# Optimization experiments

Measured on AMD Instinct MI355X. Metric: run time of the kernel, lower is better.

## Reference

```python
import jax, jax.numpy as jnp
import numpy as np

D = 1024      # dim_input
H = 16        # n_heads
DH = 64       # dim_inner
S = 1024      # current_seq
M = 1024      # pre_seq (memory)
B = 2         # batch
SCALE = 1.0 / np.sqrt(DH)


def _rel_shift(x):
    # x: [S, J, B, H]; Transformer-XL relative shift
    s, j = x.shape[0], x.shape[1]
    zero = jnp.zeros((s, 1) + x.shape[2:], x.dtype)
    x = jnp.concatenate([zero, x], axis=1)            # [S, J+1, B, H]
    x = x.reshape((j + 1, s) + x.shape[2:])[1:]        # [J, S, B, H]
    return x.reshape((s, j) + x.shape[2:])             # [S, J, B, H]


def setup_inputs() -> dict:
    key = jax.random.key(0)
    ks = jax.random.split(key, 9)
    std = 1.0 / np.sqrt(D)
    return {
        "multi_head_input": jax.random.normal(ks[0], (S, B, D), jnp.float32),
        "position_emb": jax.random.normal(ks[1], (S + M, D), jnp.float32),
        "memory": jax.random.normal(ks[2], (M, B, D), jnp.float32),
        "u": jax.random.normal(ks[3], (H, DH), jnp.float32) * 0.02,
        "v": jax.random.normal(ks[4], (H, DH), jnp.float32) * 0.02,
        "W_kv": jax.random.normal(ks[5], (D, 2 * H * DH), jnp.float32) * std,
        "W_q": jax.random.normal(ks[6], (D, H * DH), jnp.float32) * std,
        "W_pos": jax.random.normal(ks[7], (D, H * DH), jnp.float32) * std,
        "W_out": jax.random.normal(ks[8], (H * DH, D), jnp.float32) * std,
    }


def reference(multi_head_input, position_emb, memory, u, v, W_kv, W_q, W_pos, W_out):
    s = multi_head_input.shape[0]
    m = memory.shape[0]
    b = multi_head_input.shape[1]
    x_mem = jnp.concatenate([memory, multi_head_input], axis=0)   # [M+S, B, D]
    kv = x_mem @ W_kv                                              # [M+S, B, 2*H*DH]
    k, val = jnp.split(kv, 2, axis=-1)
    k = k.reshape(m + s, b, H, DH)
    val = val.reshape(m + s, b, H, DH)
    q = (multi_head_input @ W_q).reshape(s, b, H, DH)              # [S, B, H, DH]

    # content term: (q + u) . k
    content = jnp.einsum('ibhd,jbhd->ijbh', q + u, k)              # [S, M+S, B, H]
    # position term: (q + v) . r, then rel_shift
    r = (position_emb @ W_pos).reshape(m + s, H, DH)               # [M+S, H, DH]
    pos = jnp.einsum('ibhd,jhd->ijbh', q + v, r)                   # [S, M+S, B, H]
    pos = _rel_shift(pos)

    attn = jax.nn.softmax((content + pos) * SCALE, axis=1)         # [S, M+S, B, H]
    out = jnp.einsum('ijbh,jbhd->ibhd', attn, val).reshape(s, b, H * DH)
    return out @ W_out                                             # [S, B, D]
```

## Files before the change

### kernel.cpp

```cpp
#include <hip/hip_runtime.h>
#include <hip/hip_bf16.h>
#include <hip/hip_fp16.h>
#include <math.h>

#define D    1024
#define H    16
#define DH   64
#define S    1024
#define M    1024
#define B    2
#define J    2048
#define SCALE 0.125f
#define SCALE_L2E 0.18033688f

typedef __attribute__((ext_vector_type(8))) short        bf16x8;
typedef __attribute__((ext_vector_type(4))) short        s16x4;
typedef __attribute__((ext_vector_type(8))) _Float16     h16x8;
typedef __attribute__((ext_vector_type(4))) _Float16     h16x4;
typedef __attribute__((ext_vector_type(8))) unsigned short us8;
typedef __attribute__((ext_vector_type(4))) unsigned short us4;
typedef __attribute__((ext_vector_type(4))) float        f32x4;

__device__ __forceinline__ short f2bs(float f) {
    __hip_bfloat16 t = __float2bfloat16(f);
    short r; __builtin_memcpy(&r, &t, 2); return r;
}
__device__ __forceinline__ unsigned short f2bf_fast(float f) {
    unsigned int u; __builtin_memcpy(&u, &f, 4);
    return (unsigned short)((u + 0x8000u) >> 16);
}

__device__ __forceinline__ void g2l16(const short* g, short* l) {
    __builtin_amdgcn_global_load_lds(
        (const __attribute__((address_space(1))) unsigned int*)g,
        (__attribute__((address_space(3))) unsigned int*)l, 16, 0, 0);
}

__global__ __launch_bounds__(256)
void prep(const float* __restrict__ mem, const float* __restrict__ x,
          const float* __restrict__ pemb,
          const float* __restrict__ Wkv, const float* __restrict__ Wq,
          const float* __restrict__ Wpos, const float* __restrict__ Wout,
          short* __restrict__ a_bf, short* __restrict__ p_bf,
          short* __restrict__ wkvt, short* __restrict__ wqt,
          short* __restrict__ wpt,  short* __restrict__ wot)
{
    __shared__ float t[64][65];
    int blk = blockIdx.x;
    const int tid = threadIdx.x;
    if (blk < 6144) {
        const int idx = (blk * 256 + tid) * 4;
        const int TWO_M = 2 * 1024 * 1024;
        float4 v; short* dst;
        if (idx < TWO_M)          { v = *(const float4*)(mem  + idx);           dst = a_bf + idx; }
        else if (idx < 2 * TWO_M) { v = *(const float4*)(x    + idx - TWO_M);   dst = a_bf + idx; }
        else                      { v = *(const float4*)(pemb + idx - 2*TWO_M); dst = p_bf + idx - 2*TWO_M; }
        s16x4 o = { f2bs(v.x), f2bs(v.y), f2bs(v.z), f2bs(v.w) };
        *(s16x4*)dst = o;
        return;
    }
    blk -= 6144;
    const float* src; short* dst; int N, t0;
    if (blk < 512)       { src = Wkv;  dst = wkvt; N = 2048; t0 = blk; }
    else if (blk < 768)  { src = Wq;   dst = wqt;  N = 1024; t0 = blk - 512; }
    else if (blk < 1024) { src = Wpos; dst = wpt;  N = 1024; t0 = blk - 768; }
    else                 { src = Wout; dst = wot;  N = 1024; t0 = blk - 1024; }
    const int ntn = N >> 6;
    const int k0 = (t0 / ntn) * 64, n0 = (t0 % ntn) * 64;
    #pragma unroll
    for (int e = tid; e < 4096; e += 256) {
        int r = e >> 6, c = e & 63;
        t[r][c] = src[(size_t)(k0 + r) * N + n0 + c];
    }
    __syncthreads();
    #pragma unroll
    for (int e = tid; e < 4096; e += 256) {
        int nr = e >> 6, kc = e & 63;
        dst[(size_t)(n0 + nr) * 1024 + k0 + kc] = f2bs(t[kc][nr]);
    }
}

__device__ __forceinline__ void gemm_core(const short* __restrict__ A,
                                          const short* __restrict__ Bt,
                                          short* As, short* Bs,
                                          int bm0, int bn0, int tid,
                                          f32x4 acc[4][4])
{
    const int w    = tid >> 6;
    const int wy   = w >> 1, wx = w & 1;
    const int lane = tid & 63;
    const int lm   = lane & 15;
    const int lq   = lane >> 4;

    for (int k0 = 0; k0 < 1024; k0 += 64) {
        const short* Ab = A  + (size_t)bm0 * 1024 + k0;
        const short* Bb = Bt + (size_t)bn0 * 1024 + k0;
        #pragma unroll
        for (int t = 0; t < 4; ++t) {
            int s = t * 256 + tid;
            int r = s >> 3, c = s & 7;
            int cg = c ^ (r & 7);
            g2l16(Ab + r * 1024 + cg * 8, As + s * 8);
            g2l16(Bb + r * 1024 + cg * 8, Bs + s * 8);
        }
        __syncthreads();
        #pragma unroll
        for (int kk = 0; kk < 2; ++kk) {
            bf16x8 af[4], bg[4];
            #pragma unroll
            for (int r4 = 0; r4 < 4; ++r4) {
                int ar = wy * 64 + r4 * 16 + lm;
                int kc = kk * 4 + lq;
                af[r4] = *(const bf16x8*)(As + ((ar << 3) + (kc ^ (ar & 7))) * 8);
            }
            #pragma unroll
            for (int c4 = 0; c4 < 4; ++c4) {
                int br = wx * 64 + c4 * 16 + lm;
                int kc = kk * 4 + lq;
                bg[c4] = *(const bf16x8*)(Bs + ((br << 3) + (kc ^ (br & 7))) * 8);
            }
            #pragma unroll
            for (int r4 = 0; r4 < 4; ++r4)
                #pragma unroll
                for (int c4 = 0; c4 < 4; ++c4)
                    acc[r4][c4] = __builtin_amdgcn_mfma_f32_16x16x32_bf16(
                        af[r4], bg[c4], acc[r4][c4], 0, 0, 0);
        }
        __syncthreads();
    }
}

__global__ __launch_bounds__(256)
void proj_fused(const short* __restrict__ a_bf, const short* __restrict__ p_bf,
                const short* __restrict__ wkvt, const short* __restrict__ wqt,
                const short* __restrict__ wpt,
                short* __restrict__ k_bf, short* __restrict__ vt_bf,
                short* __restrict__ qu_bf, short* __restrict__ qv_bf,
                short* __restrict__ r_bf,
                const float* __restrict__ uvec, const float* __restrict__ vvec)
{
    __shared__ __align__(16) short As[128 * 64];
    __shared__ __align__(16) short Bs[128 * 64];

    int blk = (blockIdx.x & 7) * 96 + (blockIdx.x >> 3);

    int mode, bx, by;
    const short *A, *Bt;
    if (blk < 512)      { bx = blk & 15; by = blk >> 4;
                          if (bx >= 8) { mode = 4; A = wkvt; Bt = a_bf; }
                          else         { mode = 0; A = a_bf; Bt = wkvt; } }
    else if (blk < 640) { int b2 = blk - 512; mode = 1; bx = b2 & 7; by = b2 >> 3;
                          A = a_bf + (size_t)2048 * 1024; Bt = wqt; }
    else                { int b3 = blk - 640; mode = 2; bx = b3 & 7; by = b3 >> 3;
                          A = p_bf; Bt = wpt; }
    const int bn0 = (mode == 4) ? by * 128 : bx * 128;
    const int bm0 = (mode == 4) ? bx * 128 : by * 128;
    const int tid = threadIdx.x;
    const int w = tid >> 6, wy = w >> 1, wx = w & 1;
    const int lane = tid & 63, lm = lane & 15, lq = lane >> 4;

    f32x4 acc[4][4];
    #pragma unroll
    for (int r = 0; r < 4; ++r)
        #pragma unroll
        for (int c = 0; c < 4; ++c) acc[r][c] = (f32x4){0.f, 0.f, 0.f, 0.f};

    gemm_core(A, Bt, As, Bs, bm0, bn0, tid, acc);

    #pragma unroll
    for (int r4 = 0; r4 < 4; ++r4) {
        #pragma unroll
        for (int c4 = 0; c4 < 4; ++c4) {
            const int n = bn0 + wx * 64 + c4 * 16 + lm;
            float ubias = 0.f, vbias = 0.f;
            if (mode == 1) { ubias = uvec[n]; vbias = vvec[n]; }
            #pragma unroll
            for (int reg = 0; reg < 4; ++reg) {
                const int m = bm0 + wy * 64 + r4 * 16 + lq * 4 + reg;
                const float val = acc[r4][c4][reg];
                if (mode == 0) {
                    int j = m >> 1, b = m & 1;
                    int h = n >> 6, d = n & 63;
                    k_bf[(((size_t)b * H + h) * J + j) * DH + d] = f2bs(val);
                } else if (mode == 4) {
                    int n2 = m - 1024, h = n2 >> 6, d = n2 & 63;
                    int j = n >> 1, b = n & 1;
                    vt_bf[(((size_t)b * H + h) * DH + d) * J + j] = f2bs(val);
                } else if (mode == 1) {
                    int i = m >> 1, b = m & 1;
                    int h = n >> 6, d = n & 63;
                    size_t o = (((size_t)b * H + h) * S + i) * DH + d;
                    qu_bf[o] = f2bs((val + ubias) * SCALE_L2E);
                    qv_bf[o] = f2bs((val + vbias) * SCALE_L2E);
                } else {
                    int h = n >> 6, d = n & 63;
                    r_bf[((size_t)h * J + m) * DH + d] = f2bs(val);
                }
            }
        }
    }
}

__global__ __launch_bounds__(256)
void gemm_out(const short* __restrict__ A, const short* __restrict__ Bt,
              float* __restrict__ out)
{
    __shared__ __align__(16) short As[64 * 64];
    __shared__ __align__(16) short Bs[128 * 64];
    const int bn0 = blockIdx.x * 128, bm0 = blockIdx.y * 64;
    const int tid = threadIdx.x;
    const int w = tid >> 6;
    const int lane = tid & 63, lm = lane & 15, lq = lane >> 4;

    f32x4 acc[4][2];
    #pragma unroll
    for (int r = 0; r < 4; ++r)
        #pragma unroll
        for (int c = 0; c < 2; ++c) acc[r][c] = (f32x4){0.f, 0.f, 0.f, 0.f};

    for (int k0 = 0; k0 < 1024; k0 += 64) {
        const short* Ab = A  + (size_t)bm0 * 1024 + k0;
        const short* Bb = Bt + (size_t)bn0 * 1024 + k0;
        #pragma unroll
        for (int t = 0; t < 2; ++t) {
            int s = t * 256 + tid;
            int r = s >> 3, c = s & 7;
            int cg = c ^ (r & 7);
            g2l16(Ab + r * 1024 + cg * 8, As + s * 8);
        }
        #pragma unroll
        for (int t = 0; t < 4; ++t) {
            int s = t * 256 + tid;
            int r = s >> 3, c = s & 7;
            int cg = c ^ (r & 7);
            g2l16(Bb + r * 1024 + cg * 8, Bs + s * 8);
        }
        __syncthreads();
        #pragma unroll
        for (int kk = 0; kk < 2; ++kk) {
            bf16x8 af[4], bg[2];
            #pragma unroll
            for (int r4 = 0; r4 < 4; ++r4) {
                int ar = r4 * 16 + lm;
                int kc = kk * 4 + lq;
                af[r4] = *(const bf16x8*)(As + ((ar << 3) + (kc ^ (ar & 7))) * 8);
            }
            #pragma unroll
            for (int c4 = 0; c4 < 2; ++c4) {
                int br = w * 32 + c4 * 16 + lm;
                int kc = kk * 4 + lq;
                bg[c4] = *(const bf16x8*)(Bs + ((br << 3) + (kc ^ (br & 7))) * 8);
            }
            #pragma unroll
            for (int r4 = 0; r4 < 4; ++r4)
                #pragma unroll
                for (int c4 = 0; c4 < 2; ++c4)
                    acc[r4][c4] = __builtin_amdgcn_mfma_f32_16x16x32_bf16(
                        af[r4], bg[c4], acc[r4][c4], 0, 0, 0);
        }
        __syncthreads();
    }

    #pragma unroll
    for (int r4 = 0; r4 < 4; ++r4)
        #pragma unroll
        for (int c4 = 0; c4 < 2; ++c4) {
            const int n = bn0 + w * 32 + c4 * 16 + lm;
            #pragma unroll
            for (int reg = 0; reg < 4; ++reg) {
                const int m = bm0 + r4 * 16 + lq * 4 + reg;
                out[(size_t)m * 1024 + n] = acc[r4][c4][reg];
            }
        }
}

__device__ __forceinline__ int sidx(int m, int c) {
    return (m << 10) + (c ^ (m << 3));
}

__global__ __launch_bounds__(512)
void attn_mfma(const short* __restrict__ qu_bf, const short* __restrict__ qv_bf,
               const short* __restrict__ k_bf,  const short* __restrict__ vt_bf,
               const short* __restrict__ r_bf,
               float* __restrict__ opart, float* __restrict__ ml)
{
    __shared__ unsigned short sc[32 * 1024];
    __shared__ float wsum[16][2][8];
    __half* sch = (__half*)sc;
    float*  scF = (float*)sc;

    const int L   = blockIdx.x;
    const int xcd = L & 7;
    const int pp  = L >> 3;
    const int bh  = (xcd << 2) + (pp >> 6);
    const int sub = pp & 63;
    const int it  = sub >> 1;
    const int jh  = sub & 1;

    const int i0  = it * 32;
    const int cbeg = jh << 10, cend = cbeg + 1024;
    const int h   = bh & (H - 1);
    const int tid = threadIdx.x;
    const int w    = tid >> 6;
    const int lane = tid & 63;
    const int lm   = lane & 15;
    const int lq   = lane >> 4;
    const int slot = (it * 32 + bh) * 2 + jh;

    const short* qup0 = qu_bf + ((size_t)(bh * S + i0 + lm)) * DH + lq * 8;
    const short* qup1 = qup0 + 16 * DH;
    bf16x8 au00 = *(const bf16x8*)qup0,        au01 = *(const bf16x8*)(qup0 + 32);
    bf16x8 au10 = *(const bf16x8*)qup1,        au11 = *(const bf16x8*)(qup1 + 32);
    const short* qvp0 = qv_bf + ((size_t)(bh * S + i0 + lm)) * DH + lq * 8;
    const short* qvp1 = qvp0 + 16 * DH;
    bf16x8 av00 = *(const bf16x8*)qvp0,        av01 = *(const bf16x8*)(qvp0 + 32);
    bf16x8 av10 = *(const bf16x8*)qvp1,        av11 = *(const bf16x8*)(qvp1 + 32);
    int r1a = i0 + 1 + lm;  if (r1a > S - 1) r1a = S - 1;
    int r1b = i0 + 17 + lm; if (r1b > S - 1) r1b = S - 1;
    const short* qwp0 = qv_bf + ((size_t)(bh * S + r1a)) * DH + lq * 8;
    const short* qwp1 = qv_bf + ((size_t)(bh * S + r1b)) * DH + lq * 8;
    bf16x8 aw00 = *(const bf16x8*)qwp0,        aw01 = *(const bf16x8*)(qwp0 + 32);
    bf16x8 aw10 = *(const bf16x8*)qwp1,        aw11 = *(const bf16x8*)(qwp1 + 32);

    if (tid < 32) {
        int hole = i0 + tid + 1025;
        if (hole >= cbeg && hole < cend) sc[sidx(tid, hole - cbeg)] = 0;
    }

    const short* rbase = r_bf + (size_t)h * J * DH;

    {
        int tmp = cbeg + 977 - i0;
        int tlo = tmp > 0 ? ((tmp + 15) >> 4) : 0;
        int thi = (cend + 1022 - i0) >> 4; if (thi > 127) thi = 127;
        int t = tlo + w;
        if (t <= thi) {
            const short* rp = rbase + (size_t)(t * 16 + lm) * DH + lq * 8;
            bf16x8 b0 = *(const bf16x8*)rp, b1 = *(const bf16x8*)(rp + 32);
            bf16x8 p0, p1;
            if (t + 8 <= thi) {
                const short* rp2 = rbase + (size_t)((t + 8) * 16 + lm) * DH + lq * 8;
                p0 = *(const bf16x8*)rp2; p1 = *(const bf16x8*)(rp2 + 32);
            }
            for (; t <= thi; t += 8) {
                bf16x8 n0, n1;
                if (t + 16 <= thi) {
                    const short* rpn = rbase + (size_t)((t + 16) * 16 + lm) * DH + lq * 8;
                    n0 = *(const bf16x8*)rpn; n1 = *(const bf16x8*)(rpn + 32);
                }
                f32x4 c0 = {0.f,0.f,0.f,0.f}, c1 = {0.f,0.f,0.f,0.f};
                __builtin_amdgcn_s_setprio(1);
                c0 = __builtin_amdgcn_mfma_f32_16x16x32_bf16(av00, b0, c0, 0, 0, 0);
                c1 = __builtin_amdgcn_mfma_f32_16x16x32_bf16(av10, b0, c1, 0, 0, 0);
                c0 = __builtin_amdgcn_mfma_f32_16x16x32_bf16(av01, b1, c0, 0, 0, 0);
                c1 = __builtin_amdgcn_mfma_f32_16x16x32_bf16(av11, b1, c1, 0, 0, 0);
                __builtin_amdgcn_s_setprio(0);
                int cb = i0 + t * 16 + lm - 1023 - cbeg;
                int base = i0 + 16 * t - 1023;
                if (base >= cbeg && base + 46 < cend) {
                    #pragma unroll
                    for (int r = 0; r < 4; ++r) {
                        int m0 = lq * 4 + r, m1 = m0 + 16;
                        sch[sidx(m0, cb + m0)] = __float2half(c0[r]);
                        sch[sidx(m1, cb + m1)] = __float2half(c1[r]);
                    }
                } else {
                    #pragma unroll
                    for (int r = 0; r < 4; ++r) {
                        int m0 = lq * 4 + r, m1 = m0 + 16;
                        int cA = cb + m0, cB = cb + m1;
                        if (cA >= 0 && cA < 1024) sch[sidx(m0, cA)] = __float2half(c0[r]);
                        if (cB >= 0 && cB < 1024) sch[sidx(m1, cB)] = __float2half(c1[r]);
                    }
                }
                b0 = p0; b1 = p1; p0 = n0; p1 = n1;
            }
        }
    }

    {
        int tmpw = cbeg - 1072 - i0;
        int tlw = tmpw > 0 ? ((tmpw + 15) >> 4) : 0;
        int thw = (cend - 1027 - i0) >> 4; if (thw > 127) thw = 127;
        int t = tlw + w;
        if (t <= thw) {
            const short* rp = rbase + (size_t)(t * 16 + lm) * DH + lq * 8;
            bf16x8 b0 = *(const bf16x8*)rp, b1 = *(const bf16x8*)(rp + 32);
            bf16x8 p0, p1;
            if (t + 8 <= thw) {
                const short* rp2 = rbase + (size_t)((t + 8) * 16 + lm) * DH + lq * 8;
                p0 = *(const bf16x8*)rp2; p1 = *(const bf16x8*)(rp2 + 32);
            }
            for (; t <= thw; t += 8) {
                bf16x8 n0, n1;
                if (t + 16 <= thw) {
                    const short* rpn = rbase + (size_t)((t + 16) * 16 + lm) * DH + lq * 8;
                    n0 = *(const bf16x8*)rpn; n1 = *(const bf16x8*)(rpn + 32);
                }
                f32x4 c0 = {0.f,0.f,0.f,0.f}, c1 = {0.f,0.f,0.f,0.f};
                __builtin_amdgcn_s_setprio(1);
                c0 = __builtin_amdgcn_mfma_f32_16x16x32_bf16(aw00, b0, c0, 0, 0, 0);
                c1 = __builtin_amdgcn_mfma_f32_16x16x32_bf16(aw10, b0, c1, 0, 0, 0);
                c0 = __builtin_amdgcn_mfma_f32_16x16x32_bf16(aw01, b1, c0, 0, 0, 0);
                c1 = __builtin_amdgcn_mfma_f32_16x16x32_bf16(aw11, b1, c1, 0, 0, 0);
                __builtin_amdgcn_s_setprio(0);
                int cb = i0 + t * 16 + lm + 1026 - cbeg;
                int base = i0 + 16 * t + 1026;
                if (base >= cbeg && base + 46 < cend) {
                    #pragma unroll
                    for (int r = 0; r < 4; ++r) {
                        int m0 = lq * 4 + r, m1 = m0 + 16;
                        sch[sidx(m0, cb + m0)] = __float2half(c0[r]);
                        sch[sidx(m1, cb + m1)] = __float2half(c1[r]);
                    }
                } else {
                    #pragma unroll
                    for (int r = 0; r < 4; ++r) {
                        int m0 = lq * 4 + r, m1 = m0 + 16;
                        int cA = cb + m0, cB = cb + m1;
                        if (cA >= 0 && cA < 1024) sch[sidx(m0, cA)] = __float2half(c0[r]);
                        if (cB >= 0 && cB < 1024) sch[sidx(m1, cB)] = __float2half(c1[r]);
                    }
                }
                b0 = p0; b1 = p1; p0 = n0; p1 = n1;
            }
        }
    }

    const short* kbase = k_bf + (size_t)bh * J * DH;
    bf16x8 kb0, kb1, kc0, kc1;
    {
        int t0 = jh * 64 + w + 8 * ((it) & 7);
        int t1 = jh * 64 + w + 8 * ((1 + it) & 7);
        const short* kp0 = kbase + (size_t)(t0 * 16 + lm) * DH + lq * 8;
        const short* kp1 = kbase + (size_t)(t1 * 16 + lm) * DH + lq * 8;
        kb0 = *(const bf16x8*)kp0; kb1 = *(const bf16x8*)(kp0 + 32);
        kc0 = *(const bf16x8*)kp1; kc1 = *(const bf16x8*)(kp1 + 32);
    }
    __syncthreads();

    float sum0 = 0.f, sum1 = 0.f;
    #pragma unroll 1
    for (int g = 0; g < 8; ++g) {
        bf16x8 nb0, nb1;
        if (g + 2 < 8) {
            int u = jh * 64 + w + 8 * ((g + 2 + it) & 7);
            const short* np = kbase + (size_t)(u * 16 + lm) * DH + lq * 8;
            nb0 = *(const bf16x8*)np; nb1 = *(const bf16x8*)(np + 32);
        }
        int t = jh * 64 + w + 8 * ((g + it) & 7);
        int lc = t * 16 - cbeg;
        int aA = sidx(lm,      lc + lq * 4);
        int aB = sidx(lm + 16, lc + lq * 4);
        h16x4 hA = *(const h16x4*)(sc + aA);
        h16x4 hB = *(const h16x4*)(sc + aB);
        f32x4 c0, c1;
        #pragma unroll
        for (int r = 0; r < 4; ++r) { c0[r] = (float)hA[r]; c1[r] = (float)hB[r]; }
        __builtin_amdgcn_s_setprio(1);
        c0 = __builtin_amdgcn_mfma_f32_16x16x32_bf16(kb0, au00, c0, 0, 0, 0);
        c1 = __builtin_amdgcn_mfma_f32_16x16x32_bf16(kb0, au10, c1, 0, 0, 0);
        c0 = __builtin_amdgcn_mfma_f32_16x16x32_bf16(kb1, au01, c0, 0, 0, 0);
        c1 = __builtin_amdgcn_mfma_f32_16x16x32_bf16(kb1, au11, c1, 0, 0, 0);
        __builtin_amdgcn_s_setprio(0);
        us4 oA, oB;
        #pragma unroll
        for (int r = 0; r < 4; ++r) {
            float e0 = __builtin_amdgcn_exp2f(c0[r]);
            float e1 = __builtin_amdgcn_exp2f(c1[r]);
            sum0 += e0; sum1 += e1;
            oA[r] = f2bf_fast(e0);
            oB[r] = f2bf_fast(e1);
        }
        *(us4*)(sc + aA) = oA;
        *(us4*)(sc + aB) = oB;
        kb0 = kc0; kb1 = kc1; kc0 = nb0; kc1 = nb1;
    }
    sum0 += __shfl_xor(sum0, 16); sum0 += __shfl_xor(sum0, 32);
    sum1 += __shfl_xor(sum1, 16); sum1 += __shfl_xor(sum1, 32);
    if (lane < 16) { wsum[lane][0][w] = sum0; wsum[lane][1][w] = sum1; }

    const int dslice = w & 3, jq = w >> 2;
    const short* vtb = vt_bf + ((size_t)bh * DH + dslice * 16 + lm) * J + cbeg + jq * 512;
    bf16x8 cv0, cv1, cv2, cv3;
    {
        int j0 = (it & 3) * 128;
        cv0 = *(const bf16x8*)(vtb + j0 +  0 + lq * 8);
        cv1 = *(const bf16x8*)(vtb + j0 + 32 + lq * 8);
        cv2 = *(const bf16x8*)(vtb + j0 + 64 + lq * 8);
        cv3 = *(const bf16x8*)(vtb + j0 + 96 + lq * 8);
    }
    __syncthreads();

    if (tid < 32) {
        float s = 0.f;
        #pragma unroll
        for (int ww = 0; ww < 8; ++ww) s += wsum[tid & 15][tid >> 4][ww];
        ml[(size_t)slot * 64 + tid * 2]     = 0.f;
        ml[(size_t)slot * 64 + tid * 2 + 1] = s;
    }

    f32x4 pa0 = {0.f,0.f,0.f,0.f}, pa1 = {0.f,0.f,0.f,0.f};
    f32x4 pa2 = {0.f,0.f,0.f,0.f}, pa3 = {0.f,0.f,0.f,0.f};
    f32x4 pb0 = {0.f,0.f,0.f,0.f}, pb1 = {0.f,0.f,0.f,0.f};
    f32x4 pb2 = {0.f,0.f,0.f,0.f}, pb3 = {0.f,0.f,0.f,0.f};
    #pragma unroll 1
    for (int jo0 = 0; jo0 < 4; ++jo0) {
        bf16x8 nv0, nv1, nv2, nv3;
        if (jo0 < 3) {
            int jn = ((jo0 + 1 + it) & 3) * 128;
            nv0 = *(const bf16x8*)(vtb + jn +  0 + lq * 8);
            nv1 = *(const bf16x8*)(vtb + jn + 32 + lq * 8);
            nv2 = *(const bf16x8*)(vtb + jn + 64 + lq * 8);
            nv3 = *(const bf16x8*)(vtb + jn + 96 + lq * 8);
        }
        int j0 = ((jo0 + it) & 3) * 128;
        int lb = jq * 512 + j0;
        bf16x8 a0 = *(const bf16x8*)(sc + sidx(lm, lb +  0 + lq * 8));
        bf16x8 a1 = *(const bf16x8*)(sc + sidx(lm, lb + 32 + lq * 8));
        bf16x8 a2 = *(const bf16x8*)(sc + sidx(lm, lb + 64 + lq * 8));
        bf16x8 a3 = *(const bf16x8*)(sc + sidx(lm, lb + 96 + lq * 8));
        bf16x8 c0 = *(const bf16x8*)(sc + sidx(16 + lm, lb +  0 + lq * 8));
        bf16x8 c1 = *(const bf16x8*)(sc + sidx(16 + lm, lb + 32 + lq * 8));
        bf16x8 c2 = *(const bf16x8*)(sc + sidx(16 + lm, lb + 64 + lq * 8));
        bf16x8 c3 = *(const bf16x8*)(sc + sidx(16 + lm, lb + 96 + lq * 8));
        __builtin_amdgcn_s_setprio(1);
        pa0 = __builtin_amdgcn_mfma_f32_16x16x32_bf16(a0, cv0, pa0, 0, 0, 0);
        pb0 = __builtin_amdgcn_mfma_f32_16x16x32_bf16(c0, cv0, pb0, 0, 0, 0);
        pa1 = __builtin_amdgcn_mfma_f32_16x16x32_bf16(a1, cv1, pa1, 0, 0, 0);
        pb1 = __builtin_amdgcn_mfma_f32_16x16x32_bf16(c1, cv1, pb1, 0, 0, 0);
        pa2 = __builtin_amdgcn_mfma_f32_16x16x32_bf16(a2, cv2, pa2, 0, 0, 0);
        pb2 = __builtin_amdgcn_mfma_f32_16x16x32_bf16(c2, cv2, pb2, 0, 0, 0);
        pa3 = __builtin_amdgcn_mfma_f32_16x16x32_bf16(a3, cv3, pa3, 0, 0, 0);
        pb3 = __builtin_amdgcn_mfma_f32_16x16x32_bf16(c3, cv3, pb3, 0, 0, 0);
        __builtin_amdgcn_s_setprio(0);
        if (jo0 < 3) { cv0 = nv0; cv1 = nv1; cv2 = nv2; cv3 = nv3; }
    }
    __syncthreads();

    #pragma unroll
    for (int r = 0; r < 4; ++r) {
        int m0 = lq * 4 + r, m1 = m0 + 16;
        scF[jq * 2048 + m0 * 64 + dslice * 16 + lm] = pa0[r] + pa1[r] + pa2[r] + pa3[r];
        scF[jq * 2048 + m1 * 64 + dslice * 16 + lm] = pb0[r] + pb1[r] + pb2[r] + pb3[r];
    }
    __syncthreads();

    float* op = opart + (size_t)slot * 2048;
    #pragma unroll
    for (int e = tid; e < 2048; e += 512)
        op[e] = scF[e] + scF[2048 + e];
}

__global__ __launch_bounds__(256)
void attn_combine(const float* __restrict__ opart, const float* __restrict__ ml,
                  short* __restrict__ o_bf)
{
    const int blk = blockIdx.x;
    const int it = blk >> 5, bh = blk & 31;
    const int h = bh & 15, bb = bh >> 4;
    __shared__ float wgt[32][2];
    const int tid = threadIdx.x;
    if (tid < 32) {
        float m0 = ml[(size_t)(blk * 2 + 0) * 64 + tid * 2];
        float l0 = ml[(size_t)(blk * 2 + 0) * 64 + tid * 2 + 1];
        float m1 = ml[(size_t)(blk * 2 + 1) * 64 + tid * 2];
        float l1 = ml[(size_t)(blk * 2 + 1) * 64 + tid * 2 + 1];
        float mx = fmaxf(m0, m1);
        float e0 = __expf(m0 - mx), e1 = __expf(m1 - mx);
        float inv = 1.0f / (e0 * l0 + e1 * l1);
        wgt[tid][0] = e0 * inv;
        wgt[tid][1] = e1 * inv;
    }
    __syncthreads();
    const float* p0 = opart + (size_t)(blk * 2 + 0) * 2048;
    const float* p1 = opart + (size_t)(blk * 2 + 1) * 2048;
    #pragma unroll
    for (int e4 = tid; e4 < 512; e4 += 256) {
        int e = e4 * 4;
        int m = e >> 6, d = e & 63;
        float4 a = *(const float4*)(p0 + e);
        float4 b = *(const float4*)(p1 + e);
        float w0 = wgt[m][0], w1 = wgt[m][1];
        s16x4 o = { f2bs(a.x * w0 + b.x * w1), f2bs(a.y * w0 + b.y * w1),
                    f2bs(a.z * w0 + b.z * w1), f2bs(a.w * w0 + b.w * w1) };
        *(s16x4*)(o_bf + ((size_t)(it * 32 + m) * B + bb) * (H * DH) + h * DH + d) = o;
    }
}

extern "C" void kernel_launch(void* const* d_in, const int* in_sizes, int n_in,
                              void* d_out, int out_size, void* d_ws, size_t ws_size,
                              hipStream_t stream)
{
    const float* x    = (const float*)d_in[0];
    const float* pemb = (const float*)d_in[1];
    const float* mem  = (const float*)d_in[2];
    const float* u    = (const float*)d_in[3];
    const float* v    = (const float*)d_in[4];
    const float* Wkv  = (const float*)d_in[5];
    const float* Wq   = (const float*)d_in[6];
    const float* Wpos = (const float*)d_in[7];
    const float* Wout = (const float*)d_in[8];
    float* out = (float*)d_out;

    char* p = (char*)d_ws;
    short* a_bf  = (short*)p; p += (size_t)4096 * 1024 * 2;
    short* p_bf  = (short*)p; p += (size_t)2048 * 1024 * 2;
    short* wkvt  = (short*)p; p += (size_t)2048 * 1024 * 2;
    short* wqt   = (short*)p; p += (size_t)1024 * 1024 * 2;
    short* wpt   = (short*)p; p += (size_t)1024 * 1024 * 2;
    short* wot   = (short*)p; p += (size_t)1024 * 1024 * 2;
    short* k_bf  = (short*)p; p += (size_t)B * H * J * DH * 2;
    short* vt_bf = (short*)p; p += (size_t)B * H * J * DH * 2;
    short* qu_bf = (short*)p; p += (size_t)B * H * S * DH * 2;
    short* qv_bf = (short*)p; p += (size_t)B * H * S * DH * 2;
    short* r_bf  = (short*)p; p += (size_t)H * J * DH * 2;
    short* o_bf  = (short*)p;

    float* opart = (float*)d_ws;
    float* ml    = (float*)((char*)d_ws + (size_t)16 * 1024 * 1024);

    prep<<<7424, 256, 0, stream>>>(mem, x, pemb, Wkv, Wq, Wpos, Wout,
                                   a_bf, p_bf, wkvt, wqt, wpt, wot);
    proj_fused<<<768, 256, 0, stream>>>(a_bf, p_bf, wkvt, wqt, wpt,
                                        k_bf, vt_bf, qu_bf, qv_bf, r_bf, u, v);
    attn_mfma<<<2048, 512, 0, stream>>>(
        qu_bf, qv_bf, k_bf, vt_bf, r_bf, opart, ml);
    attn_combine<<<(S / 32) * B * H, 256, 0, stream>>>(opart, ml, o_bf);
    gemm_out<<<dim3(8, 32), 256, 0, stream>>>(o_bf, wot, out);
}
```

Baseline: 283.9 us.

## Fuse split-J attention halves into one block, drop combine kernel, remap gemm_out

The attention kernel now loops over both halves of the key range inside each block, accumulating the PV products and exp sums in registers. It then normalizes and writes bf16 output directly, which removes the fp32 partial buffers and the separate combine kernel launch. The grid halves to 1024 blocks, so each block does twice the serial work and there is less parallelism for latency hiding. gemm_out also gets a 1D launch with a remapped block index so that blocks sharing rows are spread across XCDs.

Measured after the change: 279.9 us. About the same (-1.4%).

```diff
diff --git a/kernel.cpp b/kernel.cpp
--- a/kernel.cpp
+++ b/kernel.cpp
@@ -207,7 +207,8 @@
 {
     __shared__ __align__(16) short As[64 * 64];
     __shared__ __align__(16) short Bs[128 * 64];
-    const int bn0 = blockIdx.x * 128, bm0 = blockIdx.y * 64;
+    const int lb = (blockIdx.x & 7) * 32 + (blockIdx.x >> 3);
+    const int bn0 = (lb & 7) * 128, bm0 = (lb >> 3) * 64;
     const int tid = threadIdx.x;
     const int w = tid >> 6;
     const int lane = tid & 63, lm = lane & 15, lq = lane >> 4;
@@ -282,260 +283,258 @@
 void attn_mfma(const short* __restrict__ qu_bf, const short* __restrict__ qv_bf,
                const short* __restrict__ k_bf,  const short* __restrict__ vt_bf,
                const short* __restrict__ r_bf,
-               float* __restrict__ opart, float* __restrict__ ml)
+               short* __restrict__ o_bf)
 {
     __shared__ unsigned short sc[32 * 1024];
     __shared__ float wsum[16][2][8];
+    __shared__ float rtot[32];
     __half* sch = (__half*)sc;
     float*  scF = (float*)sc;
 
     const int L   = blockIdx.x;
     const int xcd = L & 7;
     const int pp  = L >> 3;
-    const int bh  = (xcd << 2) + (pp >> 6);
-    const int sub = pp & 63;
-    const int it  = sub >> 1;
-    const int jh  = sub & 1;
+    const int bh  = (xcd << 2) + (pp >> 5);
+    const int it  = pp & 31;
 
     const int i0  = it * 32;
-    const int cbeg = jh << 10, cend = cbeg + 1024;
     const int h   = bh & (H - 1);
     const int tid = threadIdx.x;
     const int w    = tid >> 6;
     const int lane = tid & 63;
     const int lm   = lane & 15;
     const int lq   = lane >> 4;
-    const int slot = (it * 32 + bh) * 2 + jh;
-
-    const short* qup0 = qu_bf + ((size_t)(bh * S + i0 + lm)) * DH + lq * 8;
-    const short* qup1 = qup0 + 16 * DH;
-    bf16x8 au00 = *(const bf16x8*)qup0,        au01 = *(const bf16x8*)(qup0 + 32);
-    bf16x8 au10 = *(const bf16x8*)qup1,        au11 = *(const bf16x8*)(qup1 + 32);
-    const short* qvp0 = qv_bf + ((size_t)(bh * S + i0 + lm)) * DH + lq * 8;
-    const short* qvp1 = qvp0 + 16 * DH;
-    bf16x8 av00 = *(const bf16x8*)qvp0,        av01 = *(const bf16x8*)(qvp0 + 32);
-    bf16x8 av10 = *(const bf16x8*)qvp1,        av11 = *(const bf16x8*)(qvp1 + 32);
-    int r1a = i0 + 1 + lm;  if (r1a > S - 1) r1a = S - 1;
-    int r1b = i0 + 17 + lm; if (r1b > S - 1) r1b = S - 1;
-    const short* qwp0 = qv_bf + ((size_t)(bh * S + r1a)) * DH + lq * 8;
-    const short* qwp1 = qv_bf + ((size_t)(bh * S + r1b)) * DH + lq * 8;
-    bf16x8 aw00 = *(const bf16x8*)qwp0,        aw01 = *(const bf16x8*)(qwp0 + 32);
-    bf16x8 aw10 = *(const bf16x8*)qwp1,        aw11 = *(const bf16x8*)(qwp1 + 32);
-
-    if (tid < 32) {
-        int hole = i0 + tid + 1025;
-        if (hole >= cbeg && hole < cend) sc[sidx(tid, hole - cbeg)] = 0;
-    }
+    const int dslice = w & 3, jq = w >> 2;
 
     const short* rbase = r_bf + (size_t)h * J * DH;
-
-    {
-        int tmp = cbeg + 977 - i0;
-        int tlo = tmp > 0 ? ((tmp + 15) >> 4) : 0;
-        int thi = (cend + 1022 - i0) >> 4; if (thi > 127) thi = 127;
-        int t = tlo + w;
-        if (t <= thi) {
-            const short* rp = rbase + (size_t)(t * 16 + lm) * DH + lq * 8;
-            bf16x8 b0 = *(const bf16x8*)rp, b1 = *(const bf16x8*)(rp + 32);
-            bf16x8 p0, p1;
-            if (t + 8 <= thi) {
-                const short* rp2 = rbase + (size_t)((t + 8) * 16 + lm) * DH + lq * 8;
-                p0 = *(const bf16x8*)rp2; p1 = *(const bf16x8*)(rp2 + 32);
-            }
-            for (; t <= thi; t += 8) {
-                bf16x8 n0, n1;
-                if (t + 16 <= thi) {
-                    const short* rpn = rbase + (size_t)((t + 16) * 16 + lm) * DH + lq * 8;
-                    n0 = *(const bf16x8*)rpn; n1 = *(const bf16x8*)(rpn + 32);
-                }
-                f32x4 c0 = {0.f,0.f,0.f,0.f}, c1 = {0.f,0.f,0.f,0.f};
-                __builtin_amdgcn_s_setprio(1);
-                c0 = __builtin_amdgcn_mfma_f32_16x16x32_bf16(av00, b0, c0, 0, 0, 0);
-                c1 = __builtin_amdgcn_mfma_f32_16x16x32_bf16(av10, b0, c1, 0, 0, 0);
-                c0 = __builtin_amdgcn_mfma_f32_16x16x32_bf16(av01, b1, c0, 0, 0, 0);
-                c1 = __builtin_amdgcn_mfma_f32_16x16x32_bf16(av11, b1, c1, 0, 0, 0);
-                __builtin_amdgcn_s_setprio(0);
-                int cb = i0 + t * 16 + lm - 1023 - cbeg;
-                int base = i0 + 16 * t - 1023;
-                if (base >= cbeg && base + 46 < cend) {
-                    #pragma unroll
-                    for (int r = 0; r < 4; ++r) {
-                        int m0 = lq * 4 + r, m1 = m0 + 16;
-                        sch[sidx(m0, cb + m0)] = __float2half(c0[r]);
-                        sch[sidx(m1, cb + m1)] = __float2half(c1[r]);
-                    }
-                } else {
-                    #pragma unroll
-                    for (int r = 0; r < 4; ++r) {
-                        int m0 = lq * 4 + r, m1 = m0 + 16;
-                        int cA = cb + m0, cB = cb + m1;
-                        if (cA >= 0 && cA < 1024) sch[sidx(m0, cA)] = __float2half(c0[r]);
-                        if (cB >= 0 && cB < 1024) sch[sidx(m1, cB)] = __float2half(c1[r]);
-                    }
-                }
-                b0 = p0; b1 = p1; p0 = n0; p1 = n1;
-            }
-        }
-    }
-
-    {
-        int tmpw = cbeg - 1072 - i0;
-        int tlw = tmpw > 0 ? ((tmpw + 15) >> 4) : 0;
-        int thw = (cend - 1027 - i0) >> 4; if (thw > 127) thw = 127;
-        int t = tlw + w;
-        if (t <= thw) {
-            const short* rp = rbase + (size_t)(t * 16 + lm) * DH + lq * 8;
-            bf16x8 b0 = *(const bf16x8*)rp, b1 = *(const bf16x8*)(rp + 32);
-            bf16x8 p0, p1;
-            if (t + 8 <= thw) {
-                const short* rp2 = rbase + (size_t)((t + 8) * 16 + lm) * DH + lq * 8;
-                p0 = *(const bf16x8*)rp2; p1 = *(const bf16x8*)(rp2 + 32);
-            }
-            for (; t <= thw; t += 8) {
-                bf16x8 n0, n1;
-                if (t + 16 <= thw) {
-                    const short* rpn = rbase + (size_t)((t + 16) * 16 + lm) * DH + lq * 8;
-                    n0 = *(const bf16x8*)rpn; n1 = *(const bf16x8*)(rpn + 32);
-                }
-                f32x4 c0 = {0.f,0.f,0.f,0.f}, c1 = {0.f,0.f,0.f,0.f};
-                __builtin_amdgcn_s_setprio(1);
-                c0 = __builtin_amdgcn_mfma_f32_16x16x32_bf16(aw00, b0, c0, 0, 0, 0);
-                c1 = __builtin_amdgcn_mfma_f32_16x16x32_bf16(aw10, b0, c1, 0, 0, 0);
-                c0 = __builtin_amdgcn_mfma_f32_16x16x32_bf16(aw01, b1, c0, 0, 0, 0);
-                c1 = __builtin_amdgcn_mfma_f32_16x16x32_bf16(aw11, b1, c1, 0, 0, 0);
-                __builtin_amdgcn_s_setprio(0);
-                int cb = i0 + t * 16 + lm + 1026 - cbeg;
-                int base = i0 + 16 * t + 1026;
-                if (base >= cbeg && base + 46 < cend) {
-                    #pragma unroll
-                    for (int r = 0; r < 4; ++r) {
-                        int m0 = lq * 4 + r, m1 = m0 + 16;
-                        sch[sidx(m0, cb + m0)] = __float2half(c0[r]);
-                        sch[sidx(m1, cb + m1)] = __float2half(c1[r]);
-                    }
-                } else {
-                    #pragma unroll
-                    for (int r = 0; r < 4; ++r) {
-                        int m0 = lq * 4 + r, m1 = m0 + 16;
-                        int cA = cb + m0, cB = cb + m1;
-                        if (cA >= 0 && cA < 1024) sch[sidx(m0, cA)] = __float2half(c0[r]);
-                        if (cB >= 0 && cB < 1024) sch[sidx(m1, cB)] = __float2half(c1[r]);
-                    }
-                }
-                b0 = p0; b1 = p1; p0 = n0; p1 = n1;
-            }
-        }
-    }
-
     const short* kbase = k_bf + (size_t)bh * J * DH;
-    bf16x8 kb0, kb1, kc0, kc1;
-    {
-        int t0 = jh * 64 + w + 8 * ((it) & 7);
-        int t1 = jh * 64 + w + 8 * ((1 + it) & 7);
-        const short* kp0 = kbase + (size_t)(t0 * 16 + lm) * DH + lq * 8;
-        const short* kp1 = kbase + (size_t)(t1 * 16 + lm) * DH + lq * 8;
-        kb0 = *(const bf16x8*)kp0; kb1 = *(const bf16x8*)(kp0 + 32);
-        kc0 = *(const bf16x8*)kp1; kc1 = *(const bf16x8*)(kp1 + 32);
-    }
-    __syncthreads();
 
     float sum0 = 0.f, sum1 = 0.f;
-    #pragma unroll 1
-    for (int g = 0; g < 8; ++g) {
-        bf16x8 nb0, nb1;
-        if (g + 2 < 8) {
-            int u = jh * 64 + w + 8 * ((g + 2 + it) & 7);
-            const short* np = kbase + (size_t)(u * 16 + lm) * DH + lq * 8;
-            nb0 = *(const bf16x8*)np; nb1 = *(const bf16x8*)(np + 32);
-        }
-        int t = jh * 64 + w + 8 * ((g + it) & 7);
-        int lc = t * 16 - cbeg;
-        int aA = sidx(lm,      lc + lq * 4);
-        int aB = sidx(lm + 16, lc + lq * 4);
-        h16x4 hA = *(const h16x4*)(sc + aA);
-        h16x4 hB = *(const h16x4*)(sc + aB);
-        f32x4 c0, c1;
-        #pragma unroll
-        for (int r = 0; r < 4; ++r) { c0[r] = (float)hA[r]; c1[r] = (float)hB[r]; }
-        __builtin_amdgcn_s_setprio(1);
-        c0 = __builtin_amdgcn_mfma_f32_16x16x32_bf16(kb0, au00, c0, 0, 0, 0);
-        c1 = __builtin_amdgcn_mfma_f32_16x16x32_bf16(kb0, au10, c1, 0, 0, 0);
-        c0 = __builtin_amdgcn_mfma_f32_16x16x32_bf16(kb1, au01, c0, 0, 0, 0);
-        c1 = __builtin_amdgcn_mfma_f32_16x16x32_bf16(kb1, au11, c1, 0, 0, 0);
-        __builtin_amdgcn_s_setprio(0);
-        us4 oA, oB;
-        #pragma unroll
-        for (int r = 0; r < 4; ++r) {
-            float e0 = __builtin_amdgcn_exp2f(c0[r]);
-            float e1 = __builtin_amdgcn_exp2f(c1[r]);
-            sum0 += e0; sum1 += e1;
-            oA[r] = f2bf_fast(e0);
-            oB[r] = f2bf_fast(e1);
-        }
-        *(us4*)(sc + aA) = oA;
-        *(us4*)(sc + aB) = oB;
-        kb0 = kc0; kb1 = kc1; kc0 = nb0; kc1 = nb1;
-    }
-    sum0 += __shfl_xor(sum0, 16); sum0 += __shfl_xor(sum0, 32);
-    sum1 += __shfl_xor(sum1, 16); sum1 += __shfl_xor(sum1, 32);
-    if (lane < 16) { wsum[lane][0][w] = sum0; wsum[lane][1][w] = sum1; }
-
-    const int dslice = w & 3, jq = w >> 2;
-    const short* vtb = vt_bf + ((size_t)bh * DH + dslice * 16 + lm) * J + cbeg + jq * 512;
-    bf16x8 cv0, cv1, cv2, cv3;
-    {
-        int j0 = (it & 3) * 128;
-        cv0 = *(const bf16x8*)(vtb + j0 +  0 + lq * 8);
-        cv1 = *(const bf16x8*)(vtb + j0 + 32 + lq * 8);
-        cv2 = *(const bf16x8*)(vtb + j0 + 64 + lq * 8);
-        cv3 = *(const bf16x8*)(vtb + j0 + 96 + lq * 8);
-    }
-    __syncthreads();
-
-    if (tid < 32) {
-        float s = 0.f;
-        #pragma unroll
-        for (int ww = 0; ww < 8; ++ww) s += wsum[tid & 15][tid >> 4][ww];
-        ml[(size_t)slot * 64 + tid * 2]     = 0.f;
-        ml[(size_t)slot * 64 + tid * 2 + 1] = s;
-    }
-
     f32x4 pa0 = {0.f,0.f,0.f,0.f}, pa1 = {0.f,0.f,0.f,0.f};
     f32x4 pa2 = {0.f,0.f,0.f,0.f}, pa3 = {0.f,0.f,0.f,0.f};
     f32x4 pb0 = {0.f,0.f,0.f,0.f}, pb1 = {0.f,0.f,0.f,0.f};
     f32x4 pb2 = {0.f,0.f,0.f,0.f}, pb3 = {0.f,0.f,0.f,0.f};
+
     #pragma unroll 1
-    for (int jo0 = 0; jo0 < 4; ++jo0) {
-        bf16x8 nv0, nv1, nv2, nv3;
-        if (jo0 < 3) {
-            int jn = ((jo0 + 1 + it) & 3) * 128;
-            nv0 = *(const bf16x8*)(vtb + jn +  0 + lq * 8);
-            nv1 = *(const bf16x8*)(vtb + jn + 32 + lq * 8);
-            nv2 = *(const bf16x8*)(vtb + jn + 64 + lq * 8);
-            nv3 = *(const bf16x8*)(vtb + jn + 96 + lq * 8);
-        }
-        int j0 = ((jo0 + it) & 3) * 128;
-        int lb = jq * 512 + j0;
-        bf16x8 a0 = *(const bf16x8*)(sc + sidx(lm, lb +  0 + lq * 8));
-        bf16x8 a1 = *(const bf16x8*)(sc + sidx(lm, lb + 32 + lq * 8));
-        bf16x8 a2 = *(const bf16x8*)(sc + sidx(lm, lb + 64 + lq * 8));
-        bf16x8 a3 = *(const bf16x8*)(sc + sidx(lm, lb + 96 + lq * 8));
-        bf16x8 c0 = *(const bf16x8*)(sc + sidx(16 + lm, lb +  0 + lq * 8));
-        bf16x8 c1 = *(const bf16x8*)(sc + sidx(16 + lm, lb + 32 + lq * 8));
-        bf16x8 c2 = *(const bf16x8*)(sc + sidx(16 + lm, lb + 64 + lq * 8));
-        bf16x8 c3 = *(const bf16x8*)(sc + sidx(16 + lm, lb + 96 + lq * 8));
-        __builtin_amdgcn_s_setprio(1);
-        pa0 = __builtin_amdgcn_mfma_f32_16x16x32_bf16(a0, cv0, pa0, 0, 0, 0);
-        pb0 = __builtin_amdgcn_mfma_f32_16x16x32_bf16(c0, cv0, pb0, 0, 0, 0);
-        pa1 = __builtin_amdgcn_mfma_f32_16x16x32_bf16(a1, cv1, pa1, 0, 0, 0);
-        pb1 = __builtin_amdgcn_mfma_f32_16x16x32_bf16(c1, cv1, pb1, 0, 0, 0);
-        pa2 = __builtin_amdgcn_mfma_f32_16x16x32_bf16(a2, cv2, pa2, 0, 0, 0);
-        pb2 = __builtin_amdgcn_mfma_f32_16x16x32_bf16(c2, cv2, pb2, 0, 0, 0);
-        pa3 = __builtin_amdgcn_mfma_f32_16x16x32_bf16(a3, cv3, pa3, 0, 0, 0);
-        pb3 = __builtin_amdgcn_mfma_f32_16x16x32_bf16(c3, cv3, pb3, 0, 0, 0);
-        __builtin_amdgcn_s_setprio(0);
-        if (jo0 < 3) { cv0 = nv0; cv1 = nv1; cv2 = nv2; cv3 = nv3; }
-    }
+    for (int jh = 0; jh < 2; ++jh) {
+        const int cbeg = jh << 10, cend = cbeg + 1024;
+        if (jh) __syncthreads();
+
+        const short* qvp0 = qv_bf + ((size_t)(bh * S + i0 + lm)) * DH + lq * 8;
+        const short* qvp1 = qvp0 + 16 * DH;
+        bf16x8 av00 = *(const bf16x8*)qvp0, av01 = *(const bf16x8*)(qvp0 + 32);
+        bf16x8 av10 = *(const bf16x8*)qvp1, av11 = *(const bf16x8*)(qvp1 + 32);
+        int r1a = i0 + 1 + lm;  if (r1a > S - 1) r1a = S - 1;
+        int r1b = i0 + 17 + lm; if (r1b > S - 1) r1b = S - 1;
+        const short* qwp0 = qv_bf + ((size_t)(bh * S + r1a)) * DH + lq * 8;
+        const short* qwp1 = qv_bf + ((size_t)(bh * S + r1b)) * DH + lq * 8;
+        bf16x8 aw00 = *(const bf16x8*)qwp0, aw01 = *(const bf16x8*)(qwp0 + 32);
+        bf16x8 aw10 = *(const bf16x8*)qwp1, aw11 = *(const bf16x8*)(qwp1 + 32);
+
+        if (tid < 32) {
+            int hole = i0 + tid + 1025;
+            if (hole >= cbeg && hole < cend) sc[sidx(tid, hole - cbeg)] = 0;
+        }
+
+        {
+            int tmp = cbeg + 977 - i0;
+            int tlo = tmp > 0 ? ((tmp + 15) >> 4) : 0;
+            int thi = (cend + 1022 - i0) >> 4; if (thi > 127) thi = 127;
+            int t = tlo + w;
+            if (t <= thi) {
+                const short* rp = rbase + (size_t)(t * 16 + lm) * DH + lq * 8;
+                bf16x8 b0 = *(const bf16x8*)rp, b1 = *(const bf16x8*)(rp + 32);
+                bf16x8 p0, p1;
+                if (t + 8 <= thi) {
+                    const short* rp2 = rbase + (size_t)((t + 8) * 16 + lm) * DH + lq * 8;
+                    p0 = *(const bf16x8*)rp2; p1 = *(const bf16x8*)(rp2 + 32);
+                }
+                for (; t <= thi; t += 8) {
+                    bf16x8 n0, n1;
+                    if (t + 16 <= thi) {
+                        const short* rpn = rbase + (size_t)((t + 16) * 16 + lm) * DH + lq * 8;
+                        n0 = *(const bf16x8*)rpn; n1 = *(const bf16x8*)(rpn + 32);
+                    }
+                    f32x4 c0 = {0.f,0.f,0.f,0.f}, c1 = {0.f,0.f,0.f,0.f};
+                    __builtin_amdgcn_s_setprio(1);
+                    c0 = __builtin_amdgcn_mfma_f32_16x16x32_bf16(av00, b0, c0, 0, 0, 0);
+                    c1 = __builtin_amdgcn_mfma_f32_16x16x32_bf16(av10, b0, c1, 0, 0, 0);
+                    c0 = __builtin_amdgcn_mfma_f32_16x16x32_bf16(av01, b1, c0, 0, 0, 0);
+                    c1 = __builtin_amdgcn_mfma_f32_16x16x32_bf16(av11, b1, c1, 0, 0, 0);
+                    __builtin_amdgcn_s_setprio(0);
+                    int cb = i0 + t * 16 + lm - 1023 - cbeg;
+                    int base = i0 + 16 * t - 1023;
+                    if (base >= cbeg && base + 46 < cend) {
+                        #pragma unroll
+                        for (int r = 0; r < 4; ++r) {
+                            int m0 = lq * 4 + r, m1 = m0 + 16;
+                            sch[sidx(m0, cb + m0)] = __float2half(c0[r]);
+                            sch[sidx(m1, cb + m1)] = __float2half(c1[r]);
+                        }
+                    } else {
+                        #pragma unroll
+                        for (int r = 0; r < 4; ++r) {
+                            int m0 = lq * 4 + r, m1 = m0 + 16;
+                            int cA = cb + m0, cB = cb + m1;
+                            if (cA >= 0 && cA < 1024) sch[sidx(m0, cA)] = __float2half(c0[r]);
+                            if (cB >= 0 && cB < 1024) sch[sidx(m1, cB)] = __float2half(c1[r]);
+                        }
+                    }
+                    b0 = p0; b1 = p1; p0 = n0; p1 = n1;
+                }
+            }
+        }
+
+        {
+            int tmpw = cbeg - 1072 - i0;
+            int tlw = tmpw > 0 ? ((tmpw + 15) >> 4) : 0;
+            int thw = (cend - 1027 - i0) >> 4; if (thw > 127) thw = 127;
+            int t = tlw + w;
+            if (t <= thw) {
+                const short* rp = rbase + (size_t)(t * 16 + lm) * DH + lq * 8;
+                bf16x8 b0 = *(const bf16x8*)rp, b1 = *(const bf16x8*)(rp + 32);
+                bf16x8 p0, p1;
+                if (t + 8 <= thw) {
+                    const short* rp2 = rbase + (size_t)((t + 8) * 16 + lm) * DH + lq * 8;
+                    p0 = *(const bf16x8*)rp2; p1 = *(const bf16x8*)(rp2 + 32);
+                }
+                for (; t <= thw; t += 8) {
+                    bf16x8 n0, n1;
+                    if (t + 16 <= thw) {
+                        const short* rpn = rbase + (size_t)((t + 16) * 16 + lm) * DH + lq * 8;
+                        n0 = *(const bf16x8*)rpn; n1 = *(const bf16x8*)(rpn + 32);
+                    }
+                    f32x4 c0 = {0.f,0.f,0.f,0.f}, c1 = {0.f,0.f,0.f,0.f};
+                    __builtin_amdgcn_s_setprio(1);
+                    c0 = __builtin_amdgcn_mfma_f32_16x16x32_bf16(aw00, b0, c0, 0, 0, 0);
+                    c1 = __builtin_amdgcn_mfma_f32_16x16x32_bf16(aw10, b0, c1, 0, 0, 0);
+                    c0 = __builtin_amdgcn_mfma_f32_16x16x32_bf16(aw01, b1, c0, 0, 0, 0);
+                    c1 = __builtin_amdgcn_mfma_f32_16x16x32_bf16(aw11, b1, c1, 0, 0, 0);
+                    __builtin_amdgcn_s_setprio(0);
+                    int cb = i0 + t * 16 + lm + 1026 - cbeg;
+                    int base = i0 + 16 * t + 1026;
+                    if (base >= cbeg && base + 46 < cend) {
+                        #pragma unroll
+                        for (int r = 0; r < 4; ++r) {
+                            int m0 = lq * 4 + r, m1 = m0 + 16;
+                            sch[sidx(m0, cb + m0)] = __float2half(c0[r]);
+                            sch[sidx(m1, cb + m1)] = __float2half(c1[r]);
+                        }
+                    } else {
+                        #pragma unroll
+                        for (int r = 0; r < 4; ++r) {
+                            int m0 = lq * 4 + r, m1 = m0 + 16;
+                            int cA = cb + m0, cB = cb + m1;
+                            if (cA >= 0 && cA < 1024) sch[sidx(m0, cA)] = __float2half(c0[r]);
+                            if (cB >= 0 && cB < 1024) sch[sidx(m1, cB)] = __float2half(c1[r]);
+                        }
+                    }
+                    b0 = p0; b1 = p1; p0 = n0; p1 = n1;
+                }
+            }
+        }
+
+        bf16x8 kb0, kb1, kc0, kc1;
+        {
+            int t0 = jh * 64 + w + 8 * ((it) & 7);
+            int t1 = jh * 64 + w + 8 * ((1 + it) & 7);
+            const short* kp0 = kbase + (size_t)(t0 * 16 + lm) * DH + lq * 8;
+            const short* kp1 = kbase + (size_t)(t1 * 16 + lm) * DH + lq * 8;
+            kb0 = *(const bf16x8*)kp0; kb1 = *(const bf16x8*)(kp0 + 32);
+            kc0 = *(const bf16x8*)kp1; kc1 = *(const bf16x8*)(kp1 + 32);
+        }
+        __syncthreads();
+
+        const short* qup0 = qu_bf + ((size_t)(bh * S + i0 + lm)) * DH + lq * 8;
+        const short* qup1 = qup0 + 16 * DH;
+        bf16x8 au00 = *(const bf16x8*)qup0, au01 = *(const bf16x8*)(qup0 + 32);
+        bf16x8 au10 = *(const bf16x8*)qup1, au11 = *(const bf16x8*)(qup1 + 32);
+
+        #pragma unroll 1
+        for (int g = 0; g < 8; ++g) {
+            bf16x8 nb0, nb1;
+            if (g + 2 < 8) {
+                int u = jh * 64 + w + 8 * ((g + 2 + it) & 7);
+                const short* np = kbase + (size_t)(u * 16 + lm) * DH + lq * 8;
+                nb0 = *(const bf16x8*)np; nb1 = *(const bf16x8*)(np + 32);
+            }
+            int t = jh * 64 + w + 8 * ((g + it) & 7);
+            int lc = t * 16 - cbeg;
+            int aA = sidx(lm,      lc + lq * 4);
+            int aB = sidx(lm + 16, lc + lq * 4);
+            h16x4 hA = *(const h16x4*)(sc + aA);
+            h16x4 hB = *(const h16x4*)(sc + aB);
+            f32x4 c0, c1;
+            #pragma unroll
+            for (int r = 0; r < 4; ++r) { c0[r] = (float)hA[r]; c1[r] = (float)hB[r]; }
+            __builtin_amdgcn_s_setprio(1);
+            c0 = __builtin_amdgcn_mfma_f32_16x16x32_bf16(kb0, au00, c0, 0, 0, 0);
+            c1 = __builtin_amdgcn_mfma_f32_16x16x32_bf16(kb0, au10, c1, 0, 0, 0);
+            c0 = __builtin_amdgcn_mfma_f32_16x16x32_bf16(kb1, au01, c0, 0, 0, 0);
+            c1 = __builtin_amdgcn_mfma_f32_16x16x32_bf16(kb1, au11, c1, 0, 0, 0);
+            __builtin_amdgcn_s_setprio(0);
+            us4 oA, oB;
+            #pragma unroll
+            for (int r = 0; r < 4; ++r) {
+                float e0 = __builtin_amdgcn_exp2f(c0[r]);
+                float e1 = __builtin_amdgcn_exp2f(c1[r]);
+                sum0 += e0; sum1 += e1;
+                oA[r] = f2bf_fast(e0);
+                oB[r] = f2bf_fast(e1);
+            }
+            *(us4*)(sc + aA) = oA;
+            *(us4*)(sc + aB) = oB;
+            kb0 = kc0; kb1 = kc1; kc0 = nb0; kc1 = nb1;
+        }
+
+        const short* vtb = vt_bf + ((size_t)bh * DH + dslice * 16 + lm) * J + cbeg + jq * 512;
+        bf16x8 cv0, cv1, cv2, cv3;
+        {
+            int j0 = (it & 3) * 128;
+            cv0 = *(const bf16x8*)(vtb + j0 +  0 + lq * 8);
+            cv1 = *(const bf16x8*)(vtb + j0 + 32 + lq * 8);
+            cv2 = *(const bf16x8*)(vtb + j0 + 64 + lq * 8);
+            cv3 = *(const bf16x8*)(vtb + j0 + 96 + lq * 8);
+        }
+        __syncthreads();
+
+        #pragma unroll 1
+        for (int jo0 = 0; jo0 < 4; ++jo0) {
+            bf16x8 nv0, nv1, nv2, nv3;
+            if (jo0 < 3) {
+                int jn = ((jo0 + 1 + it) & 3) * 128;
+                nv0 = *(const bf16x8*)(vtb + jn +  0 + lq * 8);
+                nv1 = *(const bf16x8*)(vtb + jn + 32 + lq * 8);
+                nv2 = *(const bf16x8*)(vtb + jn + 64 + lq * 8);
+                nv3 = *(const bf16x8*)(vtb + jn + 96 + lq * 8);
+            }
+            int j0 = ((jo0 + it) & 3) * 128;
+            int lb = jq * 512 + j0;
+            bf16x8 a0 = *(const bf16x8*)(sc + sidx(lm, lb +  0 + lq * 8));
+            bf16x8 a1 = *(const bf16x8*)(sc + sidx(lm, lb + 32 + lq * 8));
+            bf16x8 a2 = *(const bf16x8*)(sc + sidx(lm, lb + 64 + lq * 8));
+            bf16x8 a3 = *(const bf16x8*)(sc + sidx(lm, lb + 96 + lq * 8));
+            bf16x8 c0 = *(const bf16x8*)(sc + sidx(16 + lm, lb +  0 + lq * 8));
+            bf16x8 c1 = *(const bf16x8*)(sc + sidx(16 + lm, lb + 32 + lq * 8));
+            bf16x8 c2 = *(const bf16x8*)(sc + sidx(16 + lm, lb + 64 + lq * 8));
+            bf16x8 c3 = *(const bf16x8*)(sc + sidx(16 + lm, lb + 96 + lq * 8));
+            __builtin_amdgcn_s_setprio(1);
+            pa0 = __builtin_amdgcn_mfma_f32_16x16x32_bf16(a0, cv0, pa0, 0, 0, 0);
+            pb0 = __builtin_amdgcn_mfma_f32_16x16x32_bf16(c0, cv0, pb0, 0, 0, 0);
+            pa1 = __builtin_amdgcn_mfma_f32_16x16x32_bf16(a1, cv1, pa1, 0, 0, 0);
+            pb1 = __builtin_amdgcn_mfma_f32_16x16x32_bf16(c1, cv1, pb1, 0, 0, 0);
+            pa2 = __builtin_amdgcn_mfma_f32_16x16x32_bf16(a2, cv2, pa2, 0, 0, 0);
+            pb2 = __builtin_amdgcn_mfma_f32_16x16x32_bf16(c2, cv2, pb2, 0, 0, 0);
+            pa3 = __builtin_amdgcn_mfma_f32_16x16x32_bf16(a3, cv3, pa3, 0, 0, 0);
+            pb3 = __builtin_amdgcn_mfma_f32_16x16x32_bf16(c3, cv3, pb3, 0, 0, 0);
+            __builtin_amdgcn_s_setprio(0);
+            if (jo0 < 3) { cv0 = nv0; cv1 = nv1; cv2 = nv2; cv3 = nv3; }
+        }
+    }
+
+    sum0 += __shfl_xor(sum0, 16); sum0 += __shfl_xor(sum0, 32);
+    sum1 += __shfl_xor(sum1, 16); sum1 += __shfl_xor(sum1, 32);
+    if (lane < 16) { wsum[lane][0][w] = sum0; wsum[lane][1][w] = sum1; }
     __syncthreads();
 
     #pragma unroll
@@ -544,47 +543,20 @@
         scF[jq * 2048 + m0 * 64 + dslice * 16 + lm] = pa0[r] + pa1[r] + pa2[r] + pa3[r];
         scF[jq * 2048 + m1 * 64 + dslice * 16 + lm] = pb0[r] + pb1[r] + pb2[r] + pb3[r];
     }
+    if (tid < 32) {
+        float s = 0.f;
+        #pragma unroll
+        for (int ww = 0; ww < 8; ++ww) s += wsum[tid & 15][tid >> 4][ww];
+        rtot[tid] = 1.0f / s;
+    }
     __syncthreads();
 
-    float* op = opart + (size_t)slot * 2048;
-    #pragma unroll
-    for (int e = tid; e < 2048; e += 512)
-        op[e] = scF[e] + scF[2048 + e];
-}
-
-__global__ __launch_bounds__(256)
-void attn_combine(const float* __restrict__ opart, const float* __restrict__ ml,
-                  short* __restrict__ o_bf)
-{
-    const int blk = blockIdx.x;
-    const int it = blk >> 5, bh = blk & 31;
-    const int h = bh & 15, bb = bh >> 4;
-    __shared__ float wgt[32][2];
-    const int tid = threadIdx.x;
-    if (tid < 32) {
-        float m0 = ml[(size_t)(blk * 2 + 0) * 64 + tid * 2];
-        float l0 = ml[(size_t)(blk * 2 + 0) * 64 + tid * 2 + 1];
-        float m1 = ml[(size_t)(blk * 2 + 1) * 64 + tid * 2];
-        float l1 = ml[(size_t)(blk * 2 + 1) * 64 + tid * 2 + 1];
-        float mx = fmaxf(m0, m1);
-        float e0 = __expf(m0 - mx), e1 = __expf(m1 - mx);
-        float inv = 1.0f / (e0 * l0 + e1 * l1);
-        wgt[tid][0] = e0 * inv;
-        wgt[tid][1] = e1 * inv;
-    }
-    __syncthreads();
-    const float* p0 = opart + (size_t)(blk * 2 + 0) * 2048;
-    const float* p1 = opart + (size_t)(blk * 2 + 1) * 2048;
-    #pragma unroll
-    for (int e4 = tid; e4 < 512; e4 += 256) {
-        int e = e4 * 4;
+    const int bb = bh >> 4;
+    #pragma unroll
+    for (int e = tid; e < 2048; e += 512) {
         int m = e >> 6, d = e & 63;
-        float4 a = *(const float4*)(p0 + e);
-        float4 b = *(const float4*)(p1 + e);
-        float w0 = wgt[m][0], w1 = wgt[m][1];
-        s16x4 o = { f2bs(a.x * w0 + b.x * w1), f2bs(a.y * w0 + b.y * w1),
-                    f2bs(a.z * w0 + b.z * w1), f2bs(a.w * w0 + b.w * w1) };
-        *(s16x4*)(o_bf + ((size_t)(it * 32 + m) * B + bb) * (H * DH) + h * DH + d) = o;
+        float val = (scF[e] + scF[2048 + e]) * rtot[m];
+        o_bf[((size_t)(i0 + m) * B + bb) * (H * DH) + h * DH + d] = f2bs(val);
     }
 }
 
@@ -617,15 +589,11 @@
     short* r_bf  = (short*)p; p += (size_t)H * J * DH * 2;
     short* o_bf  = (short*)p;
 
-    float* opart = (float*)d_ws;
-    float* ml    = (float*)((char*)d_ws + (size_t)16 * 1024 * 1024);
-
     prep<<<7424, 256, 0, stream>>>(mem, x, pemb, Wkv, Wq, Wpos, Wout,
                                    a_bf, p_bf, wkvt, wqt, wpt, wot);
     proj_fused<<<768, 256, 0, stream>>>(a_bf, p_bf, wkvt, wqt, wpt,
                                         k_bf, vt_bf, qu_bf, qv_bf, r_bf, u, v);
-    attn_mfma<<<2048, 512, 0, stream>>>(
-        qu_bf, qv_bf, k_bf, vt_bf, r_bf, opart, ml);
-    attn_combine<<<(S / 32) * B * H, 256, 0, stream>>>(opart, ml, o_bf);
-    gemm_out<<<dim3(8, 32), 256, 0, stream>>>(o_bf, wot, out);
-}
+    attn_mfma<<<1024, 512, 0, stream>>>(
+        qu_bf, qv_bf, k_bf, vt_bf, r_bf, o_bf);
+    gemm_out<<<256, 256, 0, stream>>>(o_bf, wot, out);
+}
```
